# Performance work log

Measured on AMD Instinct MI355X. Metric: run time of the kernel, lower is better.

Reference implementation:

```python
import jax, jax.numpy as jnp
import numpy as np

N_ITER = 50  # default n_iter of entmax.entmax_bisect


def entmax_bisect(X, alpha, n_iter=N_ITER):
    """alpha-entmax over the last axis via bisection (entmax package algorithm)."""
    d = X.shape[-1]
    am1 = alpha - 1.0
    inv = 1.0 / am1
    Xa = X * am1

    def p(z):  # clamp(z,0)**(1/(alpha-1)), grad-safe at 0
        return jnp.where(z > 0, jnp.maximum(z, 1e-30) ** inv, 0.0)

    max_val = jnp.max(Xa, axis=-1, keepdims=True)
    tau_lo = max_val - 1.0                       # _gp(1, alpha) = 1
    tau_hi = max_val - (1.0 / d) ** am1          # _gp(1/d, alpha)
    f_lo = jnp.sum(p(Xa - tau_lo), axis=-1, keepdims=True) - 1.0
    dm0 = tau_hi - tau_lo

    def body(carry, _):
        tau_lo, dm, _ = carry
        dm = dm * 0.5
        tau_m = tau_lo + dm
        f_m = jnp.sum(p(Xa - tau_m), axis=-1, keepdims=True) - 1.0
        tau_lo = jnp.where(f_m * f_lo >= 0, tau_m, tau_lo)
        return (tau_lo, dm, tau_m), None

    (_, _, tau_m), _ = jax.lax.scan(body, (tau_lo, dm0, tau_lo), None, length=n_iter)
    pm = p(Xa - tau_m)
    return pm / jnp.sum(pm, axis=-1, keepdims=True)  # ensure_sum_one=True


def setup_inputs() -> dict:
    key = jax.random.key(0)
    ks = jax.random.split(key, 10)
    b, c, e, h = 8, 2048, 64, 8
    s_in = 1.0 / np.sqrt(e)
    s_u = 1.0 / np.sqrt(h * e)
    x = jax.random.normal(ks[0], (b, c, e), jnp.float32)
    Wk = jax.random.normal(ks[1], (h * e, e), jnp.float32) * s_in
    bk = jax.random.normal(ks[2], (h * e,), jnp.float32) * 0.01
    Wq = jax.random.normal(ks[3], (h * e, e), jnp.float32) * s_in
    bq = jax.random.normal(ks[4], (h * e,), jnp.float32) * 0.01
    Wv = jax.random.normal(ks[5], (h * e, e), jnp.float32) * s_in
    bv = jax.random.normal(ks[6], (h * e,), jnp.float32) * 0.01
    Wu = jax.random.normal(ks[7], (e, h * e), jnp.float32) * s_u
    bu = jax.random.normal(ks[8], (e,), jnp.float32) * 0.01
    alpha = jnp.asarray(1.5, jnp.float32)  # learned scalar
    return dict(x=x, alpha=alpha, Wk=Wk, bk=bk, Wq=Wq, bq=bq,
                Wv=Wv, bv=bv, Wu=Wu, bu=bu)


def reference(x, alpha, Wk, bk, Wq, bq, Wv, bv, Wu, bu):
    b, c, e = x.shape
    h = Wk.shape[0] // e
    k = (x @ Wk.T + bk).reshape(b, c, h, e)
    q = (x @ Wq.T + bq).reshape(b, c, h, e)
    v = (x @ Wv.T + bv).reshape(b, c, h, e)
    # dot[b,c,i,j] = sum_h q[b,c,h,i] * k[b,c,h,j] / sqrt(e)   (per-token e x e scores)
    dot = jnp.einsum('bchi,bchj->bcij', q, k) / np.sqrt(e).astype(np.float32)
    att = entmax_bisect(dot, alpha)
    # res[b,c,h,i] = sum_j att[b,c,i,j] * v[b,c,h,j]
    res = jnp.einsum('bcij,bchj->bchi', att, v).reshape(b, c, h * e)
    return res @ Wu.T + bu
```

## Files before the change

kernel.cpp:

```cpp
#include <hip/hip_runtime.h>
#include <math.h>

#define NTOK 16384
#define EDIM 64
#define HHE  512
#define TPB  16
#define TOKPAD 260

typedef _Float16 half8 __attribute__((ext_vector_type(8)));
typedef __fp16   half2v __attribute__((ext_vector_type(2)));
typedef _Float16 f16x2 __attribute__((ext_vector_type(2)));
typedef float    floatx4 __attribute__((ext_vector_type(4)));

__device__ __forceinline__ half8 cvt8(const float4 a, const float4 b) {
    half8 h;
    h[0] = (_Float16)a.x; h[1] = (_Float16)a.y;
    h[2] = (_Float16)a.z; h[3] = (_Float16)a.w;
    h[4] = (_Float16)b.x; h[5] = (_Float16)b.y;
    h[6] = (_Float16)b.z; h[7] = (_Float16)b.w;
    return h;
}

__device__ __forceinline__ float dot2(half2v a, half2v b, float c) {
#if __has_builtin(__builtin_amdgcn_fdot2)
    return __builtin_amdgcn_fdot2(a, b, c, false);
#else
    return fmaf((float)a[0], (float)b[0], fmaf((float)a[1], (float)b[1], c));
#endif
}
__device__ __forceinline__ half2v pk(float x, float y) {
    return __builtin_amdgcn_cvt_pkrtz(x, y);
}
union h2u { half2v h; f16x2 f; unsigned int u; };

__device__ __forceinline__ unsigned pka16(unsigned a, unsigned b) {
    unsigned d;
    asm("v_pk_add_f16 %0, %1, %2" : "=v"(d) : "v"(a), "v"(b));
    return d;
}
__device__ __forceinline__ unsigned pkmax16(unsigned a, unsigned b) {
    unsigned d;
    asm("v_pk_max_f16 %0, %1, %2" : "=v"(d) : "v"(a), "v"(b));
    return d;
}
__device__ __forceinline__ unsigned pkmul16(unsigned a, unsigned b) {
    unsigned d;
    asm("v_pk_mul_f16 %0, %1, %2" : "=v"(d) : "v"(a), "v"(b));
    return d;
}
__device__ __forceinline__ unsigned pkrelu16(unsigned x, unsigned z0) {
    return pkmax16(x, z0);
}
__device__ __forceinline__ float dot2u(unsigned a, unsigned b, float c) {
    h2u ua, ub; ua.u = a; ub.u = b;
    return dot2(ua.h, ub.h, c);
}

__device__ __forceinline__ float pgen(float z, float inv) {
    return z > 0.0f ? exp2f(inv * log2f(fmaxf(z, 1e-30f))) : 0.0f;
}

__global__ __launch_bounds__(256) void cvt_fp16_kernel(
    const float* __restrict__ Wk, const float* __restrict__ Wq,
    const float* __restrict__ Wv, const float* __restrict__ Wu,
    __fp16* __restrict__ wkh, __fp16* __restrict__ wqh,
    __fp16* __restrict__ wvh, __fp16* __restrict__ wuh,
    const float* alpha_p)
{
    const int z = blockIdx.y;
    const float* src; __fp16* dst;
    float s = 1.0f;
    if      (z == 0) { src = Wk; dst = wkh; }
    else if (z == 1) { src = Wq; dst = wqh; s = (alpha_p[0] - 1.0f) * 0.125f; }
    else if (z == 2) { src = Wv; dst = wvh; }
    else             { src = Wu; dst = wuh; }
    const int idx = (blockIdx.x * 256 + threadIdx.x) * 8;
    float4 a = *(const float4*)(src + idx);
    float4 b = *(const float4*)(src + idx + 4);
    a.x *= s; a.y *= s; a.z *= s; a.w *= s;
    b.x *= s; b.y *= s; b.z *= s; b.w *= s;
    *(half8*)(dst + idx) = cvt8(a, b);
}

__global__ __launch_bounds__(256) void qkv_attn_out_kernel(
    const float* __restrict__ x,
    const __fp16* __restrict__ wkh, const float* __restrict__ bk,
    const __fp16* __restrict__ wqh, const float* __restrict__ bq,
    const __fp16* __restrict__ wvh, const float* __restrict__ bv,
    const __fp16* __restrict__ wuh, const float* __restrict__ bu,
    float* __restrict__ out, const float* alpha_p)
{
    __shared__ __align__(16) half2v qT[TPB * TOKPAD];
    __shared__ __align__(16) half2v kT[TPB * TOKPAD];
    __shared__ __align__(16) half2v vT[TPB * TOKPAD];

    const int tid  = threadIdx.x;
    const int lane = tid & 63;
    const int w    = tid >> 6;
    const int tok0 = blockIdx.x * TPB;

    const int m    = lane & 15;
    const int quad = lane >> 4;

    const float alpha = alpha_p[0];
    const float am1   = alpha - 1.0f;
    const float s_q   = am1 * 0.125f;

    const float* xrow = x + (size_t)(tok0 + m) * EDIM + quad * 8;
    half8 bfr[2];
    {
        const float4 a0 = *(const float4*)(xrow);
        const float4 a1 = *(const float4*)(xrow + 4);
        const float4 a2 = *(const float4*)(xrow + 32);
        const float4 a3 = *(const float4*)(xrow + 36);
        bfr[0] = cvt8(a0, a1);
        bfr[1] = cvt8(a2, a3);
    }

    #pragma unroll
    for (int uu = 0; uu < 3; ++uu) {
        const int unit = w * 3 + uu;
        const int z    = unit >> 2;
        const int col0 = (unit & 3) * 128;
        const __fp16* W   = (z == 0) ? wkh : (z == 1) ? wqh : wvh;
        const float* bias = (z == 0) ? bk : (z == 1) ? bq : bv;
        half2v* dstT      = (z == 0) ? kT : (z == 1) ? qT : vT;
        const float bs    = (z == 1) ? s_q : 1.0f;

        #pragma unroll
        for (int ct = 0; ct < 8; ++ct) {
            const int n = col0 + ct * 16 + m;
            const int grow = (z < 2) ? ((n & 7) * 64 + (n >> 3)) : n;
            const __fp16* wrow = W + (size_t)grow * EDIM + quad * 8;
            floatx4 acc = (floatx4){0.f, 0.f, 0.f, 0.f};
            #pragma unroll
            for (int kc = 0; kc < 2; ++kc) {
                const half8 af = *(const half8*)(wrow + kc * 32);
                acc = __builtin_amdgcn_mfma_f32_16x16x32_f16(af, bfr[kc], acc, 0, 0, 0);
            }
            h2u p0, p1;
            if (z < 2) {
                const int hbase = 4 * (quad & 1);
                const int j     = (col0 >> 3) + ct * 2 + (quad >> 1);
                float o0 = fmaf(bias[(hbase + 0) * 64 + j], bs, acc[0]);
                float o1 = fmaf(bias[(hbase + 1) * 64 + j], bs, acc[1]);
                float o2 = fmaf(bias[(hbase + 2) * 64 + j], bs, acc[2]);
                float o3 = fmaf(bias[(hbase + 3) * 64 + j], bs, acc[3]);
                p0.h = pk(o0, o1);
                p1.h = pk(o2, o3);
                uint2 st; st.x = p0.u; st.y = p1.u;
                *(uint2*)&dstT[m * TOKPAD + j * 4 + 2 * (quad & 1)] = st;
            } else {
                const int nn = col0 + ct * 16 + quad * 4;
                const int h  = nn >> 6;
                const int jj = nn & 63;
                const float4 b4 = *(const float4*)&bias[nn];
                p0.h = pk(acc[0] + b4.x, acc[1] + b4.y);
                p1.h = pk(acc[2] + b4.z, acc[3] + b4.w);
                uint2 st; st.x = p0.u; st.y = p1.u;
                *(uint2*)&dstT[m * TOKPAD + h * 32 + (jj >> 1)] = st;
            }
        }
    }
    __syncthreads();

    __fp16* resL = (__fp16*)qT;

    for (int i = 0; i < 4; ++i) {
        const int t = w * 4 + i;

        union { half8 h8; half2v h2[4]; } uq;
        uq.h8 = *(const half8*)&qT[t * TOKPAD + lane * 4];

        float inv_sum;
        half2v p2[32];

        if (am1 == 0.5f) {
            unsigned rowh[32];
            #pragma unroll
            for (int j = 0; j < 64; j += 2) {
                union { half8 h8; half2v h2[4]; } u0, u1;
                u0.h8 = *(const half8*)&kT[t * TOKPAD + j * 4];
                u1.h8 = *(const half8*)&kT[t * TOKPAD + (j + 1) * 4];
                float d0 = dot2(uq.h2[0], u0.h2[0], 0.0f);
                float d1 = dot2(uq.h2[0], u1.h2[0], 0.0f);
                d0 = dot2(uq.h2[1], u0.h2[1], d0);
                d1 = dot2(uq.h2[1], u1.h2[1], d1);
                d0 = dot2(uq.h2[2], u0.h2[2], d0);
                d1 = dot2(uq.h2[2], u1.h2[2], d1);
                d0 = dot2(uq.h2[3], u0.h2[3], d0);
                d1 = dot2(uq.h2[3], u1.h2[3], d1);
                h2u c; c.h = pk(d0, d1);
                rowh[j >> 1] = c.u;
            }

            unsigned t16[16];
            #pragma unroll
            for (int jj = 0; jj < 16; ++jj) t16[jj] = pkmax16(rowh[2*jj], rowh[2*jj+1]);
            #pragma unroll
            for (int jj = 0; jj < 8; ++jj)  t16[jj] = pkmax16(t16[jj], t16[jj+8]);
            #pragma unroll
            for (int jj = 0; jj < 4; ++jj)  t16[jj] = pkmax16(t16[jj], t16[jj+4]);
            t16[0] = pkmax16(pkmax16(t16[0], t16[1]), pkmax16(t16[2], t16[3]));
            h2u mu; mu.u = t16[0];
            const float mx = fmaxf((float)mu.f[0], (float)mu.f[1]);

            float tau_lo = mx - 1.0f;
            float dm = tau_lo - (mx - exp2f(-6.0f * am1));
            dm = -dm;
            const unsigned z0 = 0u;
            const half2v one2 = pk(1.0f, 1.0f);

            #pragma unroll
            for (int it = 0; it < 6; ++it) {
                dm *= 0.5f;
                const float tau_m = tau_lo + dm;
                h2u ntc; ntc.h = pk(-tau_m, -tau_m);
                const unsigned nt = ntc.u;
                float f0 = -1.0f, f1 = 0.0f, f2 = 0.0f, f3 = 0.0f;
                #pragma unroll
                for (int jj = 0; jj < 32; jj += 4) {
                    const unsigned a0 = pkrelu16(pka16(rowh[jj + 0], nt), z0);
                    const unsigned a1 = pkrelu16(pka16(rowh[jj + 1], nt), z0);
                    const unsigned a2 = pkrelu16(pka16(rowh[jj + 2], nt), z0);
                    const unsigned a3 = pkrelu16(pka16(rowh[jj + 3], nt), z0);
                    f0 = dot2u(a0, a0, f0);
                    f1 = dot2u(a1, a1, f1);
                    f2 = dot2u(a2, a2, f2);
                    f3 = dot2u(a3, a3, f3);
                }
                const float f = (f0 + f1) + (f2 + f3);
                tau_lo = (f >= 0.0f) ? tau_m : tau_lo;
            }
            float tau = tau_lo;
            #pragma unroll
            for (int it = 0; it < 2; ++it) {
                h2u ntc; ntc.h = pk(-tau, -tau);
                const unsigned nt = ntc.u;
                float f0 = -1.0f, f1 = 0.0f;
                float s0 = 0.0f, s1 = 0.0f;
                #pragma unroll
                for (int jj = 0; jj < 32; jj += 2) {
                    const unsigned a0 = pkrelu16(pka16(rowh[jj + 0], nt), z0);
                    const unsigned a1 = pkrelu16(pka16(rowh[jj + 1], nt), z0);
                    f0 = dot2u(a0, a0, f0);
                    f1 = dot2u(a1, a1, f1);
                    h2u ua0, ua1; ua0.u = a0; ua1.u = a1;
                    s0 = dot2(ua0.h, one2, s0);
                    s1 = dot2(ua1.h, one2, s1);
                }
                const float f = f0 + f1;
                const float s = (s0 + s1) + 1e-20f;
                tau = tau + fmaxf(f, 0.0f) * __builtin_amdgcn_rcpf(s + s);
            }
            {
                h2u ntc; ntc.h = pk(-tau, -tau);
                const unsigned nt = ntc.u;
                float s0 = 0.0f, s1 = 0.0f;
                #pragma unroll
                for (int jj = 0; jj < 32; jj += 2) {
                    const unsigned a0 = pkrelu16(pka16(rowh[jj + 0], nt), z0);
                    const unsigned a1 = pkrelu16(pka16(rowh[jj + 1], nt), z0);
                    s0 = dot2u(a0, a0, s0);
                    s1 = dot2u(a1, a1, s1);
                    h2u q0, q1;
                    q0.u = pkmul16(a0, a0);
                    q1.u = pkmul16(a1, a1);
                    p2[jj + 0] = q0.h;
                    p2[jj + 1] = q1.h;
                }
                inv_sum = __builtin_amdgcn_rcpf(s0 + s1);
            }
        } else {
            float row[64];
            #pragma unroll
            for (int j = 0; j < 64; j += 2) {
                union { half8 h8; half2v h2[4]; } u0, u1;
                u0.h8 = *(const half8*)&kT[t * TOKPAD + j * 4];
                u1.h8 = *(const half8*)&kT[t * TOKPAD + (j + 1) * 4];
                float d0 = dot2(uq.h2[0], u0.h2[0], 0.0f);
                float d1 = dot2(uq.h2[0], u1.h2[0], 0.0f);
                d0 = dot2(uq.h2[1], u0.h2[1], d0);
                d1 = dot2(uq.h2[1], u1.h2[1], d1);
                d0 = dot2(uq.h2[2], u0.h2[2], d0);
                d1 = dot2(uq.h2[2], u1.h2[2], d1);
                d0 = dot2(uq.h2[3], u0.h2[3], d0);
                d1 = dot2(uq.h2[3], u1.h2[3], d1);
                row[j] = d0; row[j + 1] = d1;
            }
            float mx = row[0];
            #pragma unroll
            for (int j = 1; j < 64; ++j) mx = fmaxf(mx, row[j]);

            float tau_lo = mx - 1.0f;
            const float tau_hi = mx - exp2f(-6.0f * am1);
            float dm = tau_hi - tau_lo;
            const float inv = 1.0f / am1;
            float tau_m = tau_lo;
            float f_lo = -1.0f;
            #pragma unroll
            for (int j = 0; j < 64; ++j) f_lo += pgen(row[j] - tau_lo, inv);
            for (int it = 0; it < 30; ++it) {
                dm *= 0.5f;
                tau_m = tau_lo + dm;
                float f = -1.0f;
                #pragma unroll
                for (int j = 0; j < 64; ++j) f += pgen(row[j] - tau_m, inv);
                tau_lo = (f * f_lo >= 0.0f) ? tau_m : tau_lo;
            }
            float s = 0.0f;
            #pragma unroll
            for (int j = 0; j < 64; ++j) {
                const float pm = pgen(row[j] - tau_m, inv);
                row[j] = pm;
                s += pm;
            }
            inv_sum = 1.0f / s;
            #pragma unroll
            for (int ii = 0; ii < 32; ++ii) p2[ii] = pk(row[2 * ii], row[2 * ii + 1]);
        }

        float acc[8];
        #pragma unroll
        for (int h = 0; h < 8; ++h) {
            float a0 = 0.0f, a1 = 0.0f;
            #pragma unroll
            for (int jc = 0; jc < 8; ++jc) {
                union { half8 h8; half2v h2[4]; } u;
                u.h8 = *(const half8*)&vT[t * TOKPAD + h * 32 + jc * 4];
                a0 = dot2(p2[jc * 4 + 0], u.h2[0], a0);
                a1 = dot2(p2[jc * 4 + 1], u.h2[1], a1);
                a0 = dot2(p2[jc * 4 + 2], u.h2[2], a0);
                a1 = dot2(p2[jc * 4 + 3], u.h2[3], a1);
            }
            acc[h] = a0 + a1;
        }
        #pragma unroll
        for (int h = 0; h < 8; ++h)
            resL[t * 520 + h * 64 + lane] = (__fp16)(acc[h] * inv_sum);
    }
    __syncthreads();

    {
        floatx4 oacc = (floatx4){0.f, 0.f, 0.f, 0.f};
        const __fp16* rrow = resL + (size_t)m * 520 + quad * 8;
        const __fp16* wrow = wuh + (size_t)(w * 16 + m) * HHE + quad * 8;
        #pragma unroll
        for (int kc = 0; kc < 16; ++kc) {
            const half8 bf = *(const half8*)(rrow + kc * 32);
            const half8 af = *(const half8*)(wrow + kc * 32);
            oacc = __builtin_amdgcn_mfma_f32_16x16x32_f16(af, bf, oacc, 0, 0, 0);
        }
        const int tok = tok0 + m;
        const int col = w * 16 + quad * 4;
        const float4 b4 = *(const float4*)&bu[col];
        float4 o;
        o.x = oacc[0] + b4.x;
        o.y = oacc[1] + b4.y;
        o.z = oacc[2] + b4.z;
        o.w = oacc[3] + b4.w;
        *(float4*)&out[(size_t)tok * 64 + col] = o;
    }
}

extern "C" void kernel_launch(void* const* d_in, const int* in_sizes, int n_in,
                              void* d_out, int out_size, void* d_ws, size_t ws_size,
                              hipStream_t stream)
{
    const float* x     = (const float*)d_in[0];
    const float* alpha = (const float*)d_in[1];
    const float* Wk    = (const float*)d_in[2];
    const float* bk    = (const float*)d_in[3];
    const float* Wq    = (const float*)d_in[4];
    const float* bq    = (const float*)d_in[5];
    const float* Wv    = (const float*)d_in[6];
    const float* bv    = (const float*)d_in[7];
    const float* Wu    = (const float*)d_in[8];
    const float* bu    = (const float*)d_in[9];
    float* out = (float*)d_out;

    __fp16* wkh  = (__fp16*)d_ws;
    __fp16* wqh  = wkh + (size_t)HHE * EDIM;
    __fp16* wvh  = wqh + (size_t)HHE * EDIM;
    __fp16* wuh  = wvh + (size_t)HHE * EDIM;

    cvt_fp16_kernel<<<dim3(16, 4), 256, 0, stream>>>(
        Wk, Wq, Wv, Wu, wkh, wqh, wvh, wuh, alpha);
    qkv_attn_out_kernel<<<NTOK / TPB, 256, 0, stream>>>(
        x, wkh, bk, wqh, bq, wvh, bv, wuh, bu, out, alpha);
}
```

Measured before the change: 157.1 us.

## Cut LDS to two buffers by staging V projection after Q is read into registers

```diff
diff --git a/kernel.cpp b/kernel.cpp
--- a/kernel.cpp
+++ b/kernel.cpp
@@ -32,6 +32,7 @@
     return __builtin_amdgcn_cvt_pkrtz(x, y);
 }
 union h2u { half2v h; f16x2 f; unsigned int u; };
+union uqu { half8 h8; half2v h2[4]; };
 
 __device__ __forceinline__ unsigned pka16(unsigned a, unsigned b) {
     unsigned d;
@@ -82,7 +83,7 @@
     *(half8*)(dst + idx) = cvt8(a, b);
 }
 
-__global__ __launch_bounds__(256) void qkv_attn_out_kernel(
+__global__ __launch_bounds__(256, 4) void qkv_attn_out_kernel(
     const float* __restrict__ x,
     const __fp16* __restrict__ wkh, const float* __restrict__ bk,
     const __fp16* __restrict__ wqh, const float* __restrict__ bq,
@@ -90,9 +91,8 @@
     const __fp16* __restrict__ wuh, const float* __restrict__ bu,
     float* __restrict__ out, const float* alpha_p)
 {
-    __shared__ __align__(16) half2v qT[TPB * TOKPAD];
+    __shared__ __align__(16) half2v bufA[TPB * TOKPAD];
     __shared__ __align__(16) half2v kT[TPB * TOKPAD];
-    __shared__ __align__(16) half2v vT[TPB * TOKPAD];
 
     const int tid  = threadIdx.x;
     const int lane = tid & 63;
@@ -118,19 +118,19 @@
     }
 
     #pragma unroll
-    for (int uu = 0; uu < 3; ++uu) {
-        const int unit = w * 3 + uu;
-        const int z    = unit >> 2;
+    for (int uu = 0; uu < 2; ++uu) {
+        const int unit = w * 2 + uu;
+        const int isq  = unit >> 2;
         const int col0 = (unit & 3) * 128;
-        const __fp16* W   = (z == 0) ? wkh : (z == 1) ? wqh : wvh;
-        const float* bias = (z == 0) ? bk : (z == 1) ? bq : bv;
-        half2v* dstT      = (z == 0) ? kT : (z == 1) ? qT : vT;
-        const float bs    = (z == 1) ? s_q : 1.0f;
+        const __fp16* W   = isq ? wqh : wkh;
+        const float* bias = isq ? bq : bk;
+        half2v* dstT      = isq ? bufA : kT;
+        const float bs    = isq ? s_q : 1.0f;
 
         #pragma unroll
         for (int ct = 0; ct < 8; ++ct) {
             const int n = col0 + ct * 16 + m;
-            const int grow = (z < 2) ? ((n & 7) * 64 + (n >> 3)) : n;
+            const int grow = (n & 7) * 64 + (n >> 3);
             const __fp16* wrow = W + (size_t)grow * EDIM + quad * 8;
             floatx4 acc = (floatx4){0.f, 0.f, 0.f, 0.f};
             #pragma unroll
@@ -138,39 +138,58 @@
                 const half8 af = *(const half8*)(wrow + kc * 32);
                 acc = __builtin_amdgcn_mfma_f32_16x16x32_f16(af, bfr[kc], acc, 0, 0, 0);
             }
+            const int hbase = 4 * (quad & 1);
+            const int j     = (col0 >> 3) + ct * 2 + (quad >> 1);
+            float o0 = fmaf(bias[(hbase + 0) * 64 + j], bs, acc[0]);
+            float o1 = fmaf(bias[(hbase + 1) * 64 + j], bs, acc[1]);
+            float o2 = fmaf(bias[(hbase + 2) * 64 + j], bs, acc[2]);
+            float o3 = fmaf(bias[(hbase + 3) * 64 + j], bs, acc[3]);
             h2u p0, p1;
-            if (z < 2) {
-                const int hbase = 4 * (quad & 1);
-                const int j     = (col0 >> 3) + ct * 2 + (quad >> 1);
-                float o0 = fmaf(bias[(hbase + 0) * 64 + j], bs, acc[0]);
-                float o1 = fmaf(bias[(hbase + 1) * 64 + j], bs, acc[1]);
-                float o2 = fmaf(bias[(hbase + 2) * 64 + j], bs, acc[2]);
-                float o3 = fmaf(bias[(hbase + 3) * 64 + j], bs, acc[3]);
-                p0.h = pk(o0, o1);
-                p1.h = pk(o2, o3);
-                uint2 st; st.x = p0.u; st.y = p1.u;
-                *(uint2*)&dstT[m * TOKPAD + j * 4 + 2 * (quad & 1)] = st;
-            } else {
-                const int nn = col0 + ct * 16 + quad * 4;
-                const int h  = nn >> 6;
-                const int jj = nn & 63;
-                const float4 b4 = *(const float4*)&bias[nn];
-                p0.h = pk(acc[0] + b4.x, acc[1] + b4.y);
-                p1.h = pk(acc[2] + b4.z, acc[3] + b4.w);
-                uint2 st; st.x = p0.u; st.y = p1.u;
-                *(uint2*)&dstT[m * TOKPAD + h * 32 + (jj >> 1)] = st;
-            }
+            p0.h = pk(o0, o1);
+            p1.h = pk(o2, o3);
+            uint2 st; st.x = p0.u; st.y = p1.u;
+            *(uint2*)&dstT[m * TOKPAD + j * 4 + 2 * (quad & 1)] = st;
         }
     }
     __syncthreads();
 
-    __fp16* resL = (__fp16*)qT;
-
+    uqu uqAll[4];
+    #pragma unroll
+    for (int i = 0; i < 4; ++i)
+        uqAll[i].h8 = *(const half8*)&bufA[(w * 4 + i) * TOKPAD + lane * 4];
+    __syncthreads();
+
+    {
+        const int col0 = w * 128;
+        #pragma unroll
+        for (int ct = 0; ct < 8; ++ct) {
+            const int n = col0 + ct * 16 + m;
+            const __fp16* wrow = wvh + (size_t)n * EDIM + quad * 8;
+            floatx4 acc = (floatx4){0.f, 0.f, 0.f, 0.f};
+            #pragma unroll
+            for (int kc = 0; kc < 2; ++kc) {
+                const half8 af = *(const half8*)(wrow + kc * 32);
+                acc = __builtin_amdgcn_mfma_f32_16x16x32_f16(af, bfr[kc], acc, 0, 0, 0);
+            }
+            const int nn = col0 + ct * 16 + quad * 4;
+            const int h  = nn >> 6;
+            const int jj = nn & 63;
+            const float4 b4 = *(const float4*)&bv[nn];
+            h2u p0, p1;
+            p0.h = pk(acc[0] + b4.x, acc[1] + b4.y);
+            p1.h = pk(acc[2] + b4.z, acc[3] + b4.w);
+            uint2 st; st.x = p0.u; st.y = p1.u;
+            *(uint2*)&bufA[m * TOKPAD + h * 32 + (jj >> 1)] = st;
+        }
+    }
+    __syncthreads();
+
+    __fp16* resL = (__fp16*)kT;
+
+    #pragma unroll
     for (int i = 0; i < 4; ++i) {
         const int t = w * 4 + i;
-
-        union { half8 h8; half2v h2[4]; } uq;
-        uq.h8 = *(const half8*)&qT[t * TOKPAD + lane * 4];
+        const uqu uq = uqAll[i];
 
         float inv_sum;
         half2v p2[32];
@@ -179,7 +198,7 @@
             unsigned rowh[32];
             #pragma unroll
             for (int j = 0; j < 64; j += 2) {
-                union { half8 h8; half2v h2[4]; } u0, u1;
+                uqu u0, u1;
                 u0.h8 = *(const half8*)&kT[t * TOKPAD + j * 4];
                 u1.h8 = *(const half8*)&kT[t * TOKPAD + (j + 1) * 4];
                 float d0 = dot2(uq.h2[0], u0.h2[0], 0.0f);
@@ -206,7 +225,7 @@
             const float mx = fmaxf((float)mu.f[0], (float)mu.f[1]);
 
             float tau_lo = mx - 1.0f;
-            float dm = tau_lo - (mx - exp2f(-6.0f * am1));
+            float dm = exp2f(-6.0f * am1) - 1.0f;
             dm = -dm;
             const unsigned z0 = 0u;
             const half2v one2 = pk(1.0f, 1.0f);
@@ -275,7 +294,7 @@
             float row[64];
             #pragma unroll
             for (int j = 0; j < 64; j += 2) {
-                union { half8 h8; half2v h2[4]; } u0, u1;
+                uqu u0, u1;
                 u0.h8 = *(const half8*)&kT[t * TOKPAD + j * 4];
                 u1.h8 = *(const half8*)&kT[t * TOKPAD + (j + 1) * 4];
                 float d0 = dot2(uq.h2[0], u0.h2[0], 0.0f);
@@ -326,8 +345,8 @@
             float a0 = 0.0f, a1 = 0.0f;
             #pragma unroll
             for (int jc = 0; jc < 8; ++jc) {
-                union { half8 h8; half2v h2[4]; } u;
-                u.h8 = *(const half8*)&vT[t * TOKPAD + h * 32 + jc * 4];
+                uqu u;
+                u.h8 = *(const half8*)&bufA[t * TOKPAD + h * 32 + jc * 4];
                 a0 = dot2(p2[jc * 4 + 0], u.h2[0], a0);
                 a1 = dot2(p2[jc * 4 + 1], u.h2[1], a1);
                 a0 = dot2(p2[jc * 4 + 2], u.h2[2], a0);
```

Result: no change. 158.1 us (+0.6%).
